# Kernel optimization log

Measured on AMD Instinct MI355X. Metric: run time of the kernel, lower is better.

Reference implementation:

```python
import jax, jax.numpy as jnp
import numpy as np

B, T, D = 4, 4096, 1024
EPS = 1e-6


def setup_inputs() -> dict:
    key = jax.random.key(0)
    ks = jax.random.split(key, 9)
    s = 0.02  # init scale for weights
    f32 = jnp.float32
    return {
        "x_seq": jax.random.normal(ks[0], (B, T, D), f32),
        "W_q": jax.random.normal(ks[1], (D, D), f32) * s,
        "b_q": jax.random.normal(ks[2], (D,), f32) * s,
        "W_k": jax.random.normal(ks[3], (D, D), f32) * s,
        "b_k": jax.random.normal(ks[4], (D,), f32) * s,
        "W_v": jax.random.normal(ks[5], (D, D), f32) * s,
        "b_v": jax.random.normal(ks[6], (D,), f32) * s,
        "W_a": jax.random.normal(ks[7], (D, D), f32) * s,
        "b_a": jax.random.normal(ks[8], (D,), f32) * s,
    }


def reference(x_seq, W_q, b_q, W_k, b_k, W_v, b_v, W_a, b_a):
    # torch nn.Linear: y = x @ W.T + b
    q = jax.nn.relu(x_seq @ W_q.T + b_q)          # [B,T,D]
    k = jax.nn.relu(x_seq @ W_k.T + b_k)          # [B,T,D]
    v = x_seq @ W_v.T + b_v                        # [B,T,D]
    A = jax.nn.sigmoid(x_seq @ W_a.T + b_a)       # [B,T,D]

    # cumprod_A[b,s,i] = prod_{u>=s} A[b,u,i], via reverse cumsum of logs
    log_g = jax.lax.cumsum(jnp.log(A + 1e-6), axis=1, reverse=True)
    wk = k * jnp.exp(log_g)                        # weighted_k [B,T,D]

    # num[b,t,j] = q_t . S_t[:,j] with S_t = cumsum_{s<=t} (wk_s outer v_s)
    # == causal-masked (q @ wk^T) @ v  (same math, no [B,T,D,D] blowup)
    scores = jnp.einsum('btd,bsd->bts', q, wk)     # [B,T,T]
    Tn = x_seq.shape[1]
    mask = jnp.tril(jnp.ones((Tn, Tn), bool))
    scores = jnp.where(mask, scores, 0.0)

    num = jnp.einsum('bts,bsd->btd', scores, v)    # [B,T,D]
    denom = scores.sum(-1, keepdims=True) + EPS    # q_t . Z_t, [B,T,1]
    return num / denom
```

## Files before the change

### kernel.cpp

```cpp
#include <hip/hip_runtime.h>

typedef unsigned short u16;
typedef unsigned int u32;

typedef __bf16 bf16x8 __attribute__((ext_vector_type(8)));
typedef float f32x4 __attribute__((ext_vector_type(4)));
typedef u16 u16x8 __attribute__((ext_vector_type(8)));

#define TSEQ 4096
#define DDIM 1024
#define NB 4
#define EPSV 1e-6f
#define CPITCH 136
#define EPITCH 264

__device__ __forceinline__ u16 f2b(float f) {
    union { float f; u32 u; } v; v.f = f;
    u32 r = v.u + 0x7FFFu + ((v.u >> 16) & 1u);
    return (u16)(r >> 16);
}
__device__ __forceinline__ float b2f(u16 h) {
    union { u32 u; float f; } v; v.u = ((u32)h) << 16; return v.f;
}
__device__ __forceinline__ u16 f2h(float f) {
    union { _Float16 h; u16 u; } v; v.h = (_Float16)f; return v.u;
}
__device__ __forceinline__ float h2f(u16 u) {
    union { u16 u; _Float16 h; } v; v.u = u; return (float)v.h;
}

__global__ __launch_bounds__(256) void k_prep(
    const float* __restrict__ x,
    const float* __restrict__ wq, const float* __restrict__ wk,
    const float* __restrict__ wv, const float* __restrict__ wa,
    const float* __restrict__ bq, const float* __restrict__ bk,
    const float* __restrict__ bv, const float* __restrict__ ba,
    u16* __restrict__ xw, u16* __restrict__ wcat, float* __restrict__ bcat,
    float* __restrict__ denom) {
    int bid = blockIdx.x, tid = threadIdx.x;
    if (bid < 1024) {
        size_t base = (size_t)bid * 4096 + tid;
#pragma unroll
        for (int k = 0; k < 16; ++k) {
            size_t f4 = base + k * 256;
            float4 f = ((const float4*)x)[f4];
            ushort4 u;
            u.x = f2b(f.x); u.y = f2b(f.y); u.z = f2b(f.z); u.w = f2b(f.w);
            *(ushort4*)(xw + f4 * 4) = u;
        }
    } else if (bid < 1280) {
        size_t base = (size_t)(bid - 1024) * 4096 + tid;
#pragma unroll
        for (int k = 0; k < 16; ++k) {
            size_t f4 = base + k * 256;
            int sel = (int)(f4 >> 18);
            const float* src = (sel == 0) ? wq : (sel == 1) ? wk : (sel == 2) ? wv : wa;
            float4 f = ((const float4*)src)[f4 & 262143];
            ushort4 u;
            u.x = f2b(f.x); u.y = f2b(f.y); u.z = f2b(f.z); u.w = f2b(f.w);
            *(ushort4*)(wcat + f4 * 4) = u;
        }
    } else if (bid == 1280) {
#pragma unroll
        for (int c = 0; c < 16; ++c) {
            int j = c * 256 + tid;
            int sel = j >> 10;
            const float* src = (sel == 0) ? bq : (sel == 1) ? bk : (sel == 2) ? bv : ba;
            bcat[j] = src[j & 1023];
        }
    } else {
        float4 z = {0.f, 0.f, 0.f, 0.f};
#pragma unroll
        for (int k = 0; k < 16; ++k)
            ((float4*)denom)[k * 256 + tid] = z;
    }
}

__device__ __forceinline__ void stage_k(u16* __restrict__ dst, const char* __restrict__ base,
                                        int ld2, int kbyte, int wid, int lane) {
#pragma unroll
    for (int c = 0; c < 4; ++c) {
        const char* g = base + c * 8 * ld2 + kbyte;
        char* l = (char*)dst + (wid * 32 + c * 8) * 128 + lane * 16;
        __builtin_amdgcn_global_load_lds((const __attribute__((address_space(1))) u32*)g,
                                         (__attribute__((address_space(3))) u32*)l, 16, 0, 0);
    }
}

__device__ __forceinline__ void mma_tile(const u16* __restrict__ As, const u16* __restrict__ Bs,
                                         f32x4 acc[4][4], int wm, int wn, int quad, int l15) {
#pragma unroll
    for (int kk = 0; kk < 64; kk += 32) {
        int cg = (kk >> 3) + quad;
        bf16x8 a[4], b[4];
#pragma unroll
        for (int i = 0; i < 4; ++i) {
            int arow = wm * 64 + i * 16 + l15;
            int brow = wn * 64 + i * 16 + l15;
            a[i] = *(const bf16x8*)(As + arow * 64 + ((cg ^ (arow & 7)) << 3));
            b[i] = *(const bf16x8*)(Bs + brow * 64 + ((cg ^ (brow & 7)) << 3));
        }
#pragma unroll
        for (int i = 0; i < 4; ++i)
#pragma unroll
            for (int j = 0; j < 4; ++j)
                acc[i][j] = __builtin_amdgcn_mfma_f32_16x16x32_bf16(a[i], b[j], acc[i][j], 0, 0, 0);
    }
}

#define STG_A(dst_d, dst_h, kofs) do { \
    const char* _g = gAt + ((dst_h) * 262144 + wid * 32768 + (kofs)); \
    char* _l = lA + ((dst_d) * 32768 + (dst_h) * 16384); \
    __builtin_amdgcn_global_load_lds((const __attribute__((address_space(1))) u32*)_g, \
        (__attribute__((address_space(3))) u32*)_l, 16, 0, 0); \
    __builtin_amdgcn_global_load_lds((const __attribute__((address_space(1))) u32*)(_g + 16384), \
        (__attribute__((address_space(3))) u32*)(_l + 1024), 16, 0, 0); \
  } while (0)

#define STG_B(dst_d, dst_h, kofs) do { \
    const char* _g = gBt + ((dst_h) * 262144 + wid * 32768 + (kofs)); \
    char* _l = lB + ((dst_d) * 32768 + (dst_h) * 16384); \
    __builtin_amdgcn_global_load_lds((const __attribute__((address_space(1))) u32*)_g, \
        (__attribute__((address_space(3))) u32*)_l, 16, 0, 0); \
    __builtin_amdgcn_global_load_lds((const __attribute__((address_space(1))) u32*)(_g + 16384), \
        (__attribute__((address_space(3))) u32*)(_l + 1024), 16, 0, 0); \
  } while (0)

#define NOP_ ((void)0)
#define VM4_ asm volatile("s_waitcnt vmcnt(4)" ::: "memory")
#define VM0_ asm volatile("s_waitcnt vmcnt(0)" ::: "memory")
#define BAR_ __builtin_amdgcn_s_barrier()
#define LGK_ asm volatile("s_waitcnt lgkmcnt(0)" ::: "memory")
#define SB0_ __builtin_amdgcn_sched_barrier(0)

#define LDA(hh, dd) do { \
    _Pragma("unroll") \
    for (int _i = 0; _i < 4; ++_i) { \
      Ar[_i][0] = *(const bf16x8*)(pA0 + ((dd) * 16384 + (hh) * 8192 + _i * 1024)); \
      Ar[_i][1] = *(const bf16x8*)(pA1 + ((dd) * 16384 + (hh) * 8192 + _i * 1024)); \
    } } while (0)

#define LDB(hh, dd) do { \
    _Pragma("unroll") \
    for (int _j = 0; _j < 2; ++_j) { \
      Br[hh][_j][0] = *(const bf16x8*)(pB0 + ((dd) * 16384 + (hh) * 8192 + _j * 1024)); \
      Br[hh][_j][1] = *(const bf16x8*)(pB1 + ((dd) * 16384 + (hh) * 8192 + _j * 1024)); \
    } } while (0)

#define MMA(qa, qb) do { \
    __builtin_amdgcn_s_setprio(1); \
    _Pragma("unroll") \
    for (int _kk = 0; _kk < 2; ++_kk) \
      _Pragma("unroll") \
      for (int _i = 0; _i < 4; ++_i) \
        _Pragma("unroll") \
        for (int _j = 0; _j < 2; ++_j) \
          acc[(qa) * 4 + _i][(qb) * 2 + _j] = __builtin_amdgcn_mfma_f32_16x16x32_bf16( \
              Ar[_i][_kk], Br[qb][_j][_kk], acc[(qa) * 4 + _i][(qb) * 2 + _j], 0, 0, 0); \
    __builtin_amdgcn_s_setprio(0); \
  } while (0)

__global__ __launch_bounds__(512, 2) void k_gemm_qkva(
    const u16* __restrict__ xw, const u16* __restrict__ wcat, const float* __restrict__ bcat,
    u16* __restrict__ qb, u16* __restrict__ kb, u16* __restrict__ vT, u16* __restrict__ gA,
    float* __restrict__ part) {
    __shared__ __align__(16) char smem[131072];
    u16* As = (u16*)smem;
    u16* Bs = (u16*)(smem + 65536);
    int tid = threadIdx.x;
    int wid = tid >> 6, lane = tid & 63;
    int wm = wid >> 2, wn = wid & 3;
    int quad = lane >> 4, l15 = lane & 15;
    int g8 = lane >> 3, hx = (lane & 7) ^ g8;
    size_t m0 = (size_t)blockIdx.x * 256, n0 = (size_t)blockIdx.y * 256;
    const char* gAp = (const char*)xw + (m0 + g8) * 2048 + hx * 16;
    const char* gBp = (const char*)wcat + (n0 + g8) * 2048 + hx * 16;
    char* lA = smem + wid * 2048 + lane * 16;
    char* lB = smem + 65536 + wid * 2048 + lane * 16;

    int x0 = (quad ^ (l15 & 7)) << 3;
    int x1 = ((quad + 4) ^ (l15 & 7)) << 3;
    const u16* pA0 = As + (wm * 64 + l15) * 64 + x0;
    const u16* pA1 = As + (wm * 64 + l15) * 64 + x1;
    const u16* pB0 = Bs + (wn * 32 + l15) * 64 + x0;
    const u16* pB1 = Bs + (wn * 32 + l15) * 64 + x1;

    f32x4 acc[8][4] = {};
    bf16x8 Ar[4][2];
    bf16x8 Br[2][2][2];

    const char* gAt = gAp;
    const char* gBt = gBp;

    STG_A(0, 0, 0); STG_A(0, 1, 0);
    STG_B(0, 0, 0); STG_B(0, 1, 0);
    STG_A(1, 0, 128); STG_B(1, 0, 128);
    VM4_;
    BAR_;

#pragma unroll 2
    for (int t = 0; t < 14; ++t) {
        int d = t & 1, dn = d ^ 1;
        LDA(0, d); LDB(0, d);
        STG_A(dn, 1, 128);
        BAR_; LGK_; SB0_; MMA(0, 0); BAR_;
        LDB(1, d);
        STG_B(dn, 1, 128);
        BAR_; LGK_; SB0_; MMA(0, 1); BAR_;
        LDA(1, d);
        STG_A(d, 0, 256);
        BAR_; LGK_; SB0_; MMA(1, 1); BAR_;
        STG_B(d, 0, 256);
        BAR_; MMA(1, 0); VM4_; BAR_;
        gAt += 128; gBt += 128;
    }
    {
        LDA(0, 0); LDB(0, 0);
        STG_A(1, 1, 128);
        BAR_; LGK_; SB0_; MMA(0, 0); BAR_;
        LDB(1, 0);
        STG_B(1, 1, 128);
        BAR_; LGK_; SB0_; MMA(0, 1); BAR_;
        LDA(1, 0);
        BAR_; LGK_; SB0_; MMA(1, 1); BAR_;
        BAR_; MMA(1, 0); VM0_; BAR_;
    }
    {
        LDA(0, 1); LDB(0, 1);
        BAR_; LGK_; SB0_; MMA(0, 0); BAR_;
        LDB(1, 1);
        BAR_; LGK_; SB0_; MMA(0, 1); BAR_;
        LDA(1, 1);
        BAR_; LGK_; SB0_; MMA(1, 1); BAR_;
        BAR_; MMA(1, 0); BAR_;
    }

    int blk = (int)(n0 >> 10), nf0 = (int)(n0 & 1023);
    int bB = (int)(m0 >> 12), t0m = (int)(m0 & 4095);
    float bias[4];
#pragma unroll
    for (int j = 0; j < 4; ++j)
        bias[j] = bcat[n0 + (size_t)((j >> 1) * 128 + wn * 32 + (j & 1) * 16 + l15)];
    u16* Cs = (u16*)smem;

#pragma unroll
    for (int h = 0; h < 2; ++h) {
        if (h) __syncthreads();
#pragma unroll
        for (int j = 0; j < 4; ++j) {
            float cs = 0.f;
            int col = (j >> 1) * 128 + wn * 32 + (j & 1) * 16 + l15;
#pragma unroll
            for (int i4 = 0; i4 < 4; ++i4) {
#pragma unroll
                for (int r = 0; r < 4; ++r) {
                    float z = acc[h * 4 + i4][j][r] + bias[j];
                    u16 o;
                    if (blk < 2) {
                        o = f2b(fmaxf(z, 0.f));
                    } else if (blk == 2) {
                        o = f2b(z);
                    } else {
                        float gg = __logf(1.f / (1.f + __expf(-z)) + 1e-6f);
                        o = f2h(gg);
                        cs += gg;
                    }
                    Cs[(wm * 64 + i4 * 16 + quad * 4 + r) * EPITCH + col] = o;
                }
            }
            if (blk == 3) {
                cs += __shfl_xor(cs, 16, 64);
                cs += __shfl_xor(cs, 32, 64);
                if (quad == 0) {
                    int chunk = (t0m >> 6) + h * 2 + wm;
                    part[((size_t)(bB * 64 + chunk) << 10) + nf0 + col] = cs;
                }
            }
        }
        __syncthreads();
        if (blk != 2) {
            u16* dst = (blk == 0) ? qb : (blk == 1) ? kb : gA;
            int lr = tid >> 2, c0 = (tid & 3) * 64;
            size_t rowo = (size_t)(m0 + h * 128 + lr) * 1024 + nf0 + c0;
#pragma unroll
            for (int i = 0; i < 8; ++i)
                *(u16x8*)(dst + rowo + i * 8) = *(const u16x8*)(Cs + lr * EPITCH + c0 + i * 8);
        } else {
            int jc = tid >> 1, th = (tid & 1) * 64;
            size_t rowo = (((size_t)(bB * 1024 + nf0 + jc)) << 12) + t0m + h * 128 + th;
#pragma unroll
            for (int i = 0; i < 8; ++i) {
                u16x8 vv;
#pragma unroll
                for (int e = 0; e < 8; ++e)
                    vv[e] = Cs[(th + i * 8 + e) * EPITCH + jc];
                *(u16x8*)(vT + rowo + i * 8) = vv;
            }
        }
    }
}

__global__ __launch_bounds__(256) void k_scan_apply(
    const u16* __restrict__ gA, const float* __restrict__ part, u16* __restrict__ kb) {
    int c = blockIdx.x, b = blockIdx.y;
    int col = blockIdx.z * 256 + threadIdx.x;
    float r = 0.f;
    for (int c2 = c + 1; c2 < 64; ++c2)
        r += part[((size_t)(b * 64 + c2) << 10) + col];
    size_t base = (((size_t)(b * TSEQ + c * 64)) << 10) + col;
#pragma unroll 4
    for (int s = 63; s >= 0; --s) {
        size_t ro = base + ((size_t)s << 10);
        r += h2f(gA[ro]);
        kb[ro] = f2b(b2f(kb[ro]) * __expf(r));
    }
}

__global__ __launch_bounds__(256) void k_scores(
    const u16* __restrict__ qb, const u16* __restrict__ wkb,
    u16* __restrict__ scores, float* __restrict__ denom) {
    int bid = blockIdx.x, b = blockIdx.y;
    int xc = bid & 7, idx = bid >> 3;
    int rs0 = xc, rs1 = 15 - xc, rs2 = 16 + xc, rs3 = 31 - xc;
    int si = 0, rem = idx;
    for (; si < 32; ++si) {
        int n = (rs0 >= si) + (rs1 >= si) + (rs2 >= si) + (rs3 >= si);
        if (rem < n) break;
        rem -= n;
    }
    int ti = rs3, cnt = 0;
    if (rs0 >= si) { if (cnt == rem) ti = rs0; ++cnt; }
    if (rs1 >= si) { if (cnt == rem) ti = rs1; ++cnt; }
    if (rs2 >= si) { if (cnt == rem) ti = rs2; ++cnt; }
    if (rs3 >= si) { if (cnt == rem) ti = rs3; ++cnt; }
    __shared__ __align__(16) char smem[CPITCH * 128 * 2];
    u16* As = (u16*)smem;
    u16* Bs = (u16*)(smem + 16384);
    int tid = threadIdx.x;
    const u16* A = qb + ((size_t)b << 22);
    const u16* Bm = wkb + ((size_t)b << 22);
    int t0 = ti * 128, s0 = si * 128;
    int wid = tid >> 6, lane = tid & 63;
    int wm = wid >> 1, wn = wid & 1, quad = lane >> 4, l15 = lane & 15;
    int hxor = (lane & 7) ^ (lane >> 3);
    const char* baA = (const char*)A + (size_t)(t0 + wid * 32 + (lane >> 3)) * 2048 + hxor * 16;
    const char* baB = (const char*)Bm + (size_t)(s0 + wid * 32 + (lane >> 3)) * 2048 + hxor * 16;
    f32x4 acc[4][4] = {};
#pragma unroll
    for (int k0 = 0; k0 < DDIM; k0 += 64) {
        stage_k(As, baA, 2048, k0 * 2, wid, lane);
        stage_k(Bs, baB, 2048, k0 * 2, wid, lane);
        __syncthreads();
        mma_tile(As, Bs, acc, wm, wn, quad, l15);
        __syncthreads();
    }
    u16* Cs = (u16*)smem;
#pragma unroll
    for (int im = 0; im < 4; ++im) {
#pragma unroll
        for (int r = 0; r < 4; ++r) {
            int trow = t0 + wm * 64 + im * 16 + quad * 4 + r;
            float rs = 0.f;
#pragma unroll
            for (int jn = 0; jn < 4; ++jn) {
                int s = s0 + wn * 64 + jn * 16 + l15;
                float val = acc[im][jn][r];
                if (s > trow) val = 0.f;
                rs += val;
                Cs[(wm * 64 + im * 16 + quad * 4 + r) * CPITCH + wn * 64 + jn * 16 + l15] = f2b(val);
            }
#pragma unroll
            for (int m = 1; m < 16; m <<= 1) rs += __shfl_xor(rs, m, 64);
            if (l15 == 0) atomicAdd(denom + (b << 12) + trow, rs);
        }
    }
    __syncthreads();
    int r = tid >> 1, ch = (tid & 1) * 64;
    size_t rowo = ((size_t)(b * TSEQ + t0 + r) << 12) + s0 + ch;
#pragma unroll
    for (int i = 0; i < 8; ++i)
        *(u16x8*)(scores + rowo + i * 8) = *(const u16x8*)(Cs + r * CPITCH + ch + i * 8);
}

__global__ __launch_bounds__(256) void k_num(
    const u16* __restrict__ scores, const u16* __restrict__ vT,
    const float* __restrict__ denom, float* __restrict__ out) {
    int ji = blockIdx.x, ti = 31 - blockIdx.y, b = blockIdx.z;
    __shared__ __align__(16) u16 As[128 * 64];
    __shared__ __align__(16) u16 Bs[128 * 64];
    int tid = threadIdx.x;
    const u16* A = scores + ((size_t)b << 24);
    const u16* Bm = vT + ((size_t)b << 22);
    int t0 = ti * 128, j0 = ji * 128;
    int wid = tid >> 6, lane = tid & 63;
    int wm = wid >> 1, wn = wid & 1, quad = lane >> 4, l15 = lane & 15;
    int hxor = (lane & 7) ^ (lane >> 3);
    const char* pA = (const char*)A + (size_t)(t0 + wid * 32 + (lane >> 3)) * 8192 + hxor * 16;
    const char* pB = (const char*)Bm + (size_t)(j0 + wid * 32 + (lane >> 3)) * 8192 + hxor * 16;
    f32x4 acc[4][4] = {};
    int kmax = (ti + 1) * 128;
    for (int k0 = 0; k0 < kmax; k0 += 128) {
        stage_k(As, pA, 8192, 0, wid, lane);
        stage_k(Bs, pB, 8192, 0, wid, lane);
        __syncthreads();
        mma_tile(As, Bs, acc, wm, wn, quad, l15);
        __syncthreads();
        stage_k(As, pA, 8192, 128, wid, lane);
        stage_k(Bs, pB, 8192, 128, wid, lane);
        __syncthreads();
        mma_tile(As, Bs, acc, wm, wn, quad, l15);
        __syncthreads();
        pA += 256; pB += 256;
    }
#pragma unroll
    for (int im = 0; im < 4; ++im) {
#pragma unroll
        for (int r = 0; r < 4; ++r) {
            int t = t0 + wm * 64 + im * 16 + quad * 4 + r;
            float den = denom[(b << 12) + t] + EPSV;
#pragma unroll
            for (int jn = 0; jn < 4; ++jn) {
                int j = j0 + wn * 64 + jn * 16 + l15;
                out[((size_t)(b * TSEQ + t) << 10) + j] = acc[im][jn][r] / den;
            }
        }
    }
}

static const size_t OFF_Q      = 0;
static const size_t OFF_WK     = 33554432;
static const size_t OFF_VT     = 67108864;
static const size_t OFF_DENOM  = 100663296;
static const size_t OFF_BCAT   = 100728832;
static const size_t OFF_XW     = 100745216;
static const size_t OFF_WCAT   = 134299648;
static const size_t OFF_GA     = 176242688;
static const size_t OFF_PART   = 243351552;
static const size_t OFF_SCORES = OFF_XW;

extern "C" void kernel_launch(void* const* d_in, const int* in_sizes, int n_in,
                              void* d_out, int out_size, void* d_ws, size_t ws_size,
                              hipStream_t stream) {
    const float* x  = (const float*)d_in[0];
    const float* Wq = (const float*)d_in[1];
    const float* bq = (const float*)d_in[2];
    const float* Wk = (const float*)d_in[3];
    const float* bk = (const float*)d_in[4];
    const float* Wv = (const float*)d_in[5];
    const float* bv = (const float*)d_in[6];
    const float* Wa = (const float*)d_in[7];
    const float* ba = (const float*)d_in[8];
    float* out = (float*)d_out;

    char* W = (char*)d_ws;
    u16* qb      = (u16*)(W + OFF_Q);
    u16* wkb     = (u16*)(W + OFF_WK);
    u16* vT      = (u16*)(W + OFF_VT);
    float* denom = (float*)(W + OFF_DENOM);
    float* bcat  = (float*)(W + OFF_BCAT);
    u16* xw      = (u16*)(W + OFF_XW);
    u16* wcat    = (u16*)(W + OFF_WCAT);
    u16* gA      = (u16*)(W + OFF_GA);
    float* part  = (float*)(W + OFF_PART);
    u16* scores  = (u16*)(W + OFF_SCORES);

    k_prep<<<1282, 256, 0, stream>>>(x, Wq, Wk, Wv, Wa, bq, bk, bv, ba, xw, wcat, bcat, denom);

    k_gemm_qkva<<<dim3(64, 16), 512, 0, stream>>>(xw, wcat, bcat, qb, wkb, vT, gA, part);

    k_scan_apply<<<dim3(64, NB, 4), 256, 0, stream>>>(gA, part, wkb);

    k_scores<<<dim3(528, NB), 256, 0, stream>>>(qb, wkb, scores, denom);

    k_num<<<dim3(8, 32, NB), 256, 0, stream>>>(scores, vT, denom, out);
}
```

Baseline: 549.0 us.

## Double-buffer A register fragments and prefetch next tile's LDS reads in GEMM

Splits the A register fragment into two halves so the next k-tile's first A/B LDS reads can be issued during the current tile's final MMA quadrant. Replaces full lgkmcnt(0) waits with partial counts and reorders the MMA quadrants and global-to-LDS staging. The aim is to hide LDS read latency behind MFMA work in the projection GEMM. In exchange it raises VGPR pressure under the 512x2 launch bounds and relies on finely tuned wait counts being correct.

```diff
diff --git a/kernel.cpp b/kernel.cpp
--- a/kernel.cpp
+++ b/kernel.cpp
@@ -127,17 +127,20 @@
   } while (0)
 
 #define NOP_ ((void)0)
+#define VM0_ asm volatile("s_waitcnt vmcnt(0)" ::: "memory")
 #define VM4_ asm volatile("s_waitcnt vmcnt(4)" ::: "memory")
-#define VM0_ asm volatile("s_waitcnt vmcnt(0)" ::: "memory")
+#define VM6_ asm volatile("s_waitcnt vmcnt(6)" ::: "memory")
 #define BAR_ __builtin_amdgcn_s_barrier()
-#define LGK_ asm volatile("s_waitcnt lgkmcnt(0)" ::: "memory")
+#define LGKM0_ asm volatile("s_waitcnt lgkmcnt(0)" ::: "memory")
+#define LGKM4_ asm volatile("s_waitcnt lgkmcnt(4)" ::: "memory")
+#define LGKM8_ asm volatile("s_waitcnt lgkmcnt(8)" ::: "memory")
 #define SB0_ __builtin_amdgcn_sched_barrier(0)
 
 #define LDA(hh, dd) do { \
     _Pragma("unroll") \
     for (int _i = 0; _i < 4; ++_i) { \
-      Ar[_i][0] = *(const bf16x8*)(pA0 + ((dd) * 16384 + (hh) * 8192 + _i * 1024)); \
-      Ar[_i][1] = *(const bf16x8*)(pA1 + ((dd) * 16384 + (hh) * 8192 + _i * 1024)); \
+      Ar[hh][_i][0] = *(const bf16x8*)(pA0 + ((dd) * 16384 + (hh) * 8192 + _i * 1024)); \
+      Ar[hh][_i][1] = *(const bf16x8*)(pA1 + ((dd) * 16384 + (hh) * 8192 + _i * 1024)); \
     } } while (0)
 
 #define LDB(hh, dd) do { \
@@ -156,8 +159,19 @@
         _Pragma("unroll") \
         for (int _j = 0; _j < 2; ++_j) \
           acc[(qa) * 4 + _i][(qb) * 2 + _j] = __builtin_amdgcn_mfma_f32_16x16x32_bf16( \
-              Ar[_i][_kk], Br[qb][_j][_kk], acc[(qa) * 4 + _i][(qb) * 2 + _j], 0, 0, 0); \
+              Ar[qa][_i][_kk], Br[qb][_j][_kk], acc[(qa) * 4 + _i][(qb) * 2 + _j], 0, 0, 0); \
     __builtin_amdgcn_s_setprio(0); \
+  } while (0)
+
+#define TILE(d, dn, S0, S1, S2, S3, W2, W3) do { \
+    LDB(1, d); S0; SB0_; \
+    BAR_; LGKM4_; SB0_; MMA(0, 0); BAR_; \
+    LDA(1, d); S1; SB0_; \
+    BAR_; LGKM8_; SB0_; MMA(0, 1); BAR_; \
+    S2; SB0_; \
+    BAR_; LGKM0_; SB0_; MMA(1, 0); W2; BAR_; \
+    LDA(0, dn); LDB(0, dn); S3; SB0_; \
+    BAR_; MMA(1, 1); W3; BAR_; \
   } while (0)
 
 __global__ __launch_bounds__(512, 2) void k_gemm_qkva(
@@ -186,53 +200,39 @@
     const u16* pB1 = Bs + (wn * 32 + l15) * 64 + x1;
 
     f32x4 acc[8][4] = {};
-    bf16x8 Ar[4][2];
+    bf16x8 Ar[2][4][2];
     bf16x8 Br[2][2][2];
 
     const char* gAt = gAp;
     const char* gBt = gBp;
 
-    STG_A(0, 0, 0); STG_A(0, 1, 0);
-    STG_B(0, 0, 0); STG_B(0, 1, 0);
+    STG_A(0, 0, 0); STG_B(0, 0, 0);
+    STG_A(0, 1, 0); STG_B(0, 1, 0);
     STG_A(1, 0, 128); STG_B(1, 0, 128);
     VM4_;
     BAR_;
+    LDA(0, 0); LDB(0, 0);
 
 #pragma unroll 2
     for (int t = 0; t < 14; ++t) {
         int d = t & 1, dn = d ^ 1;
-        LDA(0, d); LDB(0, d);
-        STG_A(dn, 1, 128);
-        BAR_; LGK_; SB0_; MMA(0, 0); BAR_;
-        LDB(1, d);
-        STG_B(dn, 1, 128);
-        BAR_; LGK_; SB0_; MMA(0, 1); BAR_;
-        LDA(1, d);
-        STG_A(d, 0, 256);
-        BAR_; LGK_; SB0_; MMA(1, 1); BAR_;
-        STG_B(d, 0, 256);
-        BAR_; MMA(1, 0); VM4_; BAR_;
+        TILE(d, dn,
+             STG_A(dn, 1, 128), STG_B(dn, 1, 128),
+             STG_A(d, 0, 256), STG_B(d, 0, 256),
+             VM6_, VM4_);
         gAt += 128; gBt += 128;
     }
+    TILE(0, 1,
+         STG_A(1, 1, 128), STG_B(1, 1, 128),
+         NOP_, NOP_,
+         VM4_, VM0_);
     {
-        LDA(0, 0); LDB(0, 0);
-        STG_A(1, 1, 128);
-        BAR_; LGK_; SB0_; MMA(0, 0); BAR_;
-        LDB(1, 0);
-        STG_B(1, 1, 128);
-        BAR_; LGK_; SB0_; MMA(0, 1); BAR_;
-        LDA(1, 0);
-        BAR_; LGK_; SB0_; MMA(1, 1); BAR_;
-        BAR_; MMA(1, 0); VM0_; BAR_;
-    }
-    {
-        LDA(0, 1); LDB(0, 1);
-        BAR_; LGK_; SB0_; MMA(0, 0); BAR_;
         LDB(1, 1);
-        BAR_; LGK_; SB0_; MMA(0, 1); BAR_;
+        BAR_; LGKM4_; SB0_; MMA(0, 0); BAR_;
         LDA(1, 1);
-        BAR_; LGK_; SB0_; MMA(1, 1); BAR_;
-        BAR_; MMA(1, 0); BAR_;
+        BAR_; LGKM8_; SB0_; MMA(0, 1); BAR_;
+        BAR_; LGKM0_; SB0_; MMA(1, 0); BAR_;
+        BAR_; MMA(1, 1); BAR_;
     }
 
     int blk = (int)(n0 >> 10), nf0 = (int)(n0 & 1023);
```

Result: slower. 562.6 us (+2.5%).
